# Kernel optimization log

Measured on AMD Instinct MI355X. Metric: run time of the kernel, lower is better.

Reference implementation:

```python
import jax, jax.numpy as jnp
import numpy as np

H = 256          # decoder_size
V = 3            # vocab_size
MAX_LENGTH = 64


def lstm_cell(x, h, c, Wih, Whh, b):
    # PyTorch gate order: i, f, g, o
    g = x @ Wih.T + h @ Whh.T + b
    i, f, gg, o = jnp.split(g, 4, axis=-1)
    c = jax.nn.sigmoid(f) * c + jax.nn.sigmoid(i) * jnp.tanh(gg)
    h = jax.nn.sigmoid(o) * jnp.tanh(c)
    return h, c


def setup_inputs() -> dict:
    key = jax.random.key(0)
    ks = jax.random.split(key, 16)
    T, B, F = 512, 32, 1024
    s = 1.0 / np.sqrt(H)
    u = lambda k, shape: jax.random.uniform(k, shape, jnp.float32, -s, s)
    return dict(
        cnn_feats=jax.random.normal(ks[0], (T, B, F), jnp.float32),
        # bidirectional encoder LSTM (1 layer)
        enc_Wih_f=u(ks[1], (4 * H, F)), enc_Whh_f=u(ks[2], (4 * H, H)), enc_b_f=u(ks[3], (4 * H,)),
        enc_Wih_b=u(ks[4], (4 * H, F)), enc_Whh_b=u(ks[5], (4 * H, H)), enc_b_b=u(ks[6], (4 * H,)),
        # 2-layer decoder LSTM
        dec_Wih0=u(ks[7], (4 * H, H)), dec_Whh0=u(ks[8], (4 * H, H)), dec_b0=u(ks[9], (4 * H,)),
        dec_Wih1=u(ks[10], (4 * H, H)), dec_Whh1=u(ks[11], (4 * H, H)), dec_b1=u(ks[12], (4 * H,)),
        # per-step output projection
        lin_W=u(ks[13], (V, H)), lin_b=u(ks[14], (V,)),
    )


def _forward(cnn_feats, enc_Wih_f, enc_Whh_f, enc_b_f, enc_Wih_b, enc_Whh_b, enc_b_b,
             dec_Wih0, dec_Whh0, dec_b0, dec_Wih1, dec_Whh1, dec_b1, lin_W, lin_b):
    B = cnn_feats.shape[1]
    z = jnp.zeros((B, H), cnn_feats.dtype)

    def run_dir(seq, Wih, Whh, b):
        def step(carry, x):
            h, c = lstm_cell(x, carry[0], carry[1], Wih, Whh, b)
            return (h, c), None
        (h, c), _ = jax.lax.scan(step, (z, z), seq)
        return h, c

    # encoder final states: fwd over seq, bwd over reversed seq
    hf, cf = run_dir(cnn_feats, enc_Wih_f, enc_Whh_f, enc_b_f)
    hb, cb = run_dir(cnn_feats[::-1], enc_Wih_b, enc_Whh_b, enc_b_b)

    # decoder: layer0 init = fwd-dir state, layer1 init = bwd-dir state
    def dstep(carry, _):
        x, h0, c0, h1, c1 = carry
        h0, c0 = lstm_cell(x, h0, c0, dec_Wih0, dec_Whh0, dec_b0)
        h1, c1 = lstm_cell(h0, h1, c1, dec_Wih1, dec_Whh1, dec_b1)
        y = h1 @ lin_W.T + lin_b
        return (h1, h0, c0, h1, c1), y

    _, ys = jax.lax.scan(dstep, (z, hf, cf, hb, cb), None, length=MAX_LENGTH)
    return ys  # (MAX_LENGTH, B, V)


def reference(cnn_feats, enc_Wih_f, enc_Whh_f, enc_b_f, enc_Wih_b, enc_Whh_b, enc_b_b,
              dec_Wih0, dec_Whh0, dec_b0, dec_Wih1, dec_Whh1, dec_b1, lin_W, lin_b):
    return _forward(cnn_feats, enc_Wih_f, enc_Whh_f, enc_b_f, enc_Wih_b, enc_Whh_b, enc_b_b,
                    dec_Wih0, dec_Whh0, dec_b0, dec_Wih1, dec_Whh1, dec_b1, lin_W, lin_b)
```

## Files before the change

kernel.cpp:

```cpp
#include <hip/hip_runtime.h>
#include <stdint.h>
#include <stddef.h>

typedef __attribute__((ext_vector_type(8))) short  short8;
typedef __attribute__((ext_vector_type(4))) float  floatx4;
typedef __attribute__((ext_vector_type(4))) unsigned int u32x4;
typedef unsigned long long u64;

#define SENT 0xAAAAAAAAAAAAAAAAull

static __device__ __forceinline__ float b2f(uint16_t h) {
  union { uint32_t u; float f; } v; v.u = ((uint32_t)h) << 16; return v.f;
}
static __device__ __forceinline__ uint16_t f2b(float f) {
  union { float f; uint32_t u; } v; v.f = f;
  uint32_t u = v.u;
  uint32_t r = u + 0x7FFFu + ((u >> 16) & 1u);
  return (uint16_t)(r >> 16);
}
static __device__ __forceinline__ float sigm(float x)  { return 1.0f / (1.0f + __expf(-x)); }
static __device__ __forceinline__ float tanh_f(float x){ return 1.0f - 2.0f / (1.0f + __expf(2.0f * x)); }

static __device__ __forceinline__ floatx4 mfma16(short8 a, short8 b, floatx4 c) {
  return __builtin_amdgcn_mfma_f32_16x16x32_bf16(a, b, c, 0, 0, 0);
}
static __device__ __forceinline__ short8 cvt8(const float* p) {
  short8 r;
  #pragma unroll
  for (int i = 0; i < 8; ++i) r[i] = (short)f2b(p[i]);
  return r;
}

static __device__ __forceinline__ void st_h64(uint16_t* p, u64 v) {
  __hip_atomic_store((u64*)p, v, __ATOMIC_RELAXED, __HIP_MEMORY_SCOPE_AGENT);
}
static __device__ __forceinline__ u64 ld_h64(const u64* p) {
  return __hip_atomic_load(p, __ATOMIC_RELAXED, __HIP_MEMORY_SCOPE_AGENT);
}
static __device__ __forceinline__ bool frag_ok(u32x4 v) {
  const u64 lo = ((u64)v[1] << 32) | v[0];
  const u64 hi = ((u64)v[3] << 32) | v[2];
  return (lo != SENT) & (hi != SENT);
}
static __device__ __forceinline__ void ld8x16(const uint16_t* p, u32x4* o) {
  asm volatile(
      "global_load_dwordx4 %0, %8, off sc0 sc1\n\t"
      "global_load_dwordx4 %1, %8, off offset:64 sc0 sc1\n\t"
      "global_load_dwordx4 %2, %8, off offset:128 sc0 sc1\n\t"
      "global_load_dwordx4 %3, %8, off offset:192 sc0 sc1\n\t"
      "global_load_dwordx4 %4, %8, off offset:256 sc0 sc1\n\t"
      "global_load_dwordx4 %5, %8, off offset:320 sc0 sc1\n\t"
      "global_load_dwordx4 %6, %8, off offset:384 sc0 sc1\n\t"
      "global_load_dwordx4 %7, %8, off offset:448 sc0 sc1\n\t"
      "s_waitcnt vmcnt(0)"
      : "=&v"(o[0]), "=&v"(o[1]), "=&v"(o[2]), "=&v"(o[3]),
        "=&v"(o[4]), "=&v"(o[5]), "=&v"(o[6]), "=&v"(o[7])
      : "v"(p)
      : "memory");
}
static __device__ __forceinline__ void ld16x16(const uint16_t* pa, const uint16_t* pb,
                                               u32x4* oa, u32x4* ob) {
  asm volatile(
      "global_load_dwordx4 %0, %16, off sc0 sc1\n\t"
      "global_load_dwordx4 %1, %16, off offset:64 sc0 sc1\n\t"
      "global_load_dwordx4 %2, %16, off offset:128 sc0 sc1\n\t"
      "global_load_dwordx4 %3, %16, off offset:192 sc0 sc1\n\t"
      "global_load_dwordx4 %4, %16, off offset:256 sc0 sc1\n\t"
      "global_load_dwordx4 %5, %16, off offset:320 sc0 sc1\n\t"
      "global_load_dwordx4 %6, %16, off offset:384 sc0 sc1\n\t"
      "global_load_dwordx4 %7, %16, off offset:448 sc0 sc1\n\t"
      "global_load_dwordx4 %8, %17, off sc0 sc1\n\t"
      "global_load_dwordx4 %9, %17, off offset:64 sc0 sc1\n\t"
      "global_load_dwordx4 %10, %17, off offset:128 sc0 sc1\n\t"
      "global_load_dwordx4 %11, %17, off offset:192 sc0 sc1\n\t"
      "global_load_dwordx4 %12, %17, off offset:256 sc0 sc1\n\t"
      "global_load_dwordx4 %13, %17, off offset:320 sc0 sc1\n\t"
      "global_load_dwordx4 %14, %17, off offset:384 sc0 sc1\n\t"
      "global_load_dwordx4 %15, %17, off offset:448 sc0 sc1\n\t"
      "s_waitcnt vmcnt(0)"
      : "=&v"(oa[0]), "=&v"(oa[1]), "=&v"(oa[2]), "=&v"(oa[3]),
        "=&v"(oa[4]), "=&v"(oa[5]), "=&v"(oa[6]), "=&v"(oa[7]),
        "=&v"(ob[0]), "=&v"(ob[1]), "=&v"(ob[2]), "=&v"(ob[3]),
        "=&v"(ob[4]), "=&v"(ob[5]), "=&v"(ob[6]), "=&v"(ob[7])
      : "v"(pa), "v"(pb)
      : "memory");
}
static __device__ __forceinline__ void valve8(const uint16_t* p, u32x4* o) {
  const u64* q = (const u64*)p;
  #pragma unroll
  for (int k = 0; k < 8; ++k) {
    u64 a = ld_h64(q + k * 8), c = ld_h64(q + k * 8 + 1);
    o[k][0] = (unsigned)a; o[k][1] = (unsigned)(a >> 32);
    o[k][2] = (unsigned)c; o[k][3] = (unsigned)(c >> 32);
  }
}
static __device__ __forceinline__ void poll8f(const uint16_t* p, u32x4* o) {
  int it = 0;
  for (;;) {
    if ((++it & 1023) == 0) valve8(p, o); else ld8x16(p, o);
    bool ok = true;
    #pragma unroll
    for (int k = 0; k < 8; ++k) ok &= frag_ok(o[k]);
    if (ok) break;
    __builtin_amdgcn_s_sleep(1);
  }
}
static __device__ __forceinline__ void poll16f(const uint16_t* pa, const uint16_t* pb,
                                               u32x4* oa, u32x4* ob) {
  int it = 0;
  for (;;) {
    if ((++it & 1023) == 0) { valve8(pa, oa); valve8(pb, ob); }
    else ld16x16(pa, pb, oa, ob);
    bool ok = true;
    #pragma unroll
    for (int k = 0; k < 8; ++k) ok &= frag_ok(oa[k]) & frag_ok(ob[k]);
    if (ok) break;
    __builtin_amdgcn_s_sleep(1);
  }
}

#define H 256
#define FH 1024
#define BATCH 32
#define TSEQ 512
#define DSTEPS 64
#define ERING 8

__global__ __launch_bounds__(256) void gemm_xw(
    const float* __restrict__ A, const float* __restrict__ W,
    const float* __restrict__ bias, void* __restrict__ Cout, int out_f32)
{
  const int K = 1024, N = 1024;
  __shared__ uint16_t Ah[64 * 40], Al[64 * 40];
  __shared__ uint16_t Wh[64 * 40], Wl[64 * 40];
  const int m0 = blockIdx.x * 64;
  const int n0 = blockIdx.y * 64;
  const int tid = threadIdx.x;
  const int lane = tid & 63, w = tid >> 6;
  const int wm = w & 1, wn = w >> 1;
  const int l15 = lane & 15, q4 = lane >> 4;
  const int ldrow = tid >> 2, ldk = (tid & 3) * 8;

  floatx4 acc[2][2];
  for (int i = 0; i < 2; ++i) for (int j = 0; j < 2; ++j) acc[i][j] = (floatx4){0.f,0.f,0.f,0.f};

  for (int kb = 0; kb < K; kb += 32) {
    float aa[8], ww[8];
    {
      const float4* ap = (const float4*)(A + (size_t)(m0 + ldrow) * K + kb + ldk);
      const float4* wp = (const float4*)(W + (size_t)(n0 + ldrow) * K + kb + ldk);
      *(float4*)(aa) = ap[0]; *(float4*)(aa + 4) = ap[1];
      *(float4*)(ww) = wp[0]; *(float4*)(ww + 4) = wp[1];
    }
    short8 ah, al, wh, wl;
    #pragma unroll
    for (int i = 0; i < 8; ++i) {
      uint16_t h = f2b(aa[i]); ah[i] = (short)h; al[i] = (short)f2b(aa[i] - b2f(h));
      uint16_t g = f2b(ww[i]); wh[i] = (short)g; wl[i] = (short)f2b(ww[i] - b2f(g));
    }
    __syncthreads();
    *(short8*)(Ah + ldrow * 40 + ldk) = ah;
    *(short8*)(Al + ldrow * 40 + ldk) = al;
    *(short8*)(Wh + ldrow * 40 + ldk) = wh;
    *(short8*)(Wl + ldrow * 40 + ldk) = wl;
    __syncthreads();
    short8 afh[2], afl[2], bfh[2], bfl[2];
    #pragma unroll
    for (int mt = 0; mt < 2; ++mt) {
      afh[mt] = *(const short8*)(Ah + (wm * 32 + mt * 16 + l15) * 40 + q4 * 8);
      afl[mt] = *(const short8*)(Al + (wm * 32 + mt * 16 + l15) * 40 + q4 * 8);
    }
    #pragma unroll
    for (int nt = 0; nt < 2; ++nt) {
      bfh[nt] = *(const short8*)(Wh + (wn * 32 + nt * 16 + l15) * 40 + q4 * 8);
      bfl[nt] = *(const short8*)(Wl + (wn * 32 + nt * 16 + l15) * 40 + q4 * 8);
    }
    #pragma unroll
    for (int mt = 0; mt < 2; ++mt)
      #pragma unroll
      for (int nt = 0; nt < 2; ++nt) {
        acc[mt][nt] = mfma16(afh[mt], bfh[nt], acc[mt][nt]);
        acc[mt][nt] = mfma16(afh[mt], bfl[nt], acc[mt][nt]);
        acc[mt][nt] = mfma16(afl[mt], bfh[nt], acc[mt][nt]);
      }
  }
  #pragma unroll
  for (int mt = 0; mt < 2; ++mt)
    #pragma unroll
    for (int nt = 0; nt < 2; ++nt) {
      const int col = n0 + wn * 32 + nt * 16 + l15;
      const float bv = bias[col];
      #pragma unroll
      for (int r = 0; r < 4; ++r) {
        const int row = m0 + wm * 32 + mt * 16 + q4 * 4 + r;
        const float v = acc[mt][nt][r] + bv;
        if (out_f32) ((float*)Cout)[(size_t)row * N + col] = v;
        else         ((uint16_t*)Cout)[(size_t)row * N + col] = f2b(v);
      }
    }
}

__global__ __launch_bounds__(256, 1) void enc_rnn(
    const void* __restrict__ XgF, const void* __restrict__ XgB, int xg_f32,
    const float* __restrict__ WhhF, const float* __restrict__ WhhB,
    uint16_t* __restrict__ hslots,
    uint16_t* __restrict__ hfin, float* __restrict__ cfin)
{
  const int d = blockIdx.x >> 3, q = blockIdx.x & 7;
  const void*  Xg  = d ? XgB : XgF;
  const float* Whh = d ? WhhB : WhhF;
  uint16_t* hsl = hslots + d * (ERING * BATCH * H);
  const int jOff = q * 32;
  const int tid = threadIdx.x, lane = tid & 63, w = tid >> 6;
  const int tt = w & 1, nt = w >> 1, l15 = lane & 15, q4 = lane >> 4;
  const int b = nt * 16 + l15;
  const int jg = jOff + tt * 16 + q4 * 4;

  short8 Af[4][8];
  #pragma unroll
  for (int g = 0; g < 4; ++g) {
    const int grow = g * H + jOff + tt * 16 + l15;
    #pragma unroll
    for (int ks = 0; ks < 8; ++ks)
      Af[g][ks] = cvt8(Whh + (size_t)grow * H + ks * 32 + q4 * 8);
  }

  float cc[4] = {0.f, 0.f, 0.f, 0.f};
  union HV { uint16_t u16[4]; u64 v; } hv; hv.v = 0ull;

  float xvf[16];
  u64   xvb[4];
  auto ldx = [&](int s2) {
    const int t2 = d ? (TSEQ - 1 - s2) : s2;
    const size_t bas = (size_t)(t2 * BATCH + b) * FH + jg;
    if (xg_f32) {
      const float* xp = (const float*)Xg + bas;
      *(float4*)(xvf + 0)  = *(const float4*)(xp);
      *(float4*)(xvf + 4)  = *(const float4*)(xp + H);
      *(float4*)(xvf + 8)  = *(const float4*)(xp + 2 * H);
      *(float4*)(xvf + 12) = *(const float4*)(xp + 3 * H);
    } else {
      const uint16_t* xp = (const uint16_t*)Xg + bas;
      xvb[0] = *(const u64*)(xp);
      xvb[1] = *(const u64*)(xp + H);
      xvb[2] = *(const u64*)(xp + 2 * H);
      xvb[3] = *(const u64*)(xp + 3 * H);
    }
  };
  ldx(0);

  for (int s = 0; s < TSEQ; ++s) {
    floatx4 a0 = {0.f,0.f,0.f,0.f}, a1 = a0, a2 = a0, a3 = a0;
    if (s > 0) {
      u32x4 pol[8];
      const uint16_t* ps = hsl + ((s - 1) & (ERING - 1)) * (BATCH * H) + b * H + q4 * 8;
      poll8f(ps, pol);
      #pragma unroll
      for (int ks = 0; ks < 8; ++ks) {
        short8 bfv = *(short8*)&pol[ks];
        a0 = mfma16(Af[0][ks], bfv, a0);
        a1 = mfma16(Af[1][ks], bfv, a1);
        a2 = mfma16(Af[2][ks], bfv, a2);
        a3 = mfma16(Af[3][ks], bfv, a3);
      }
    }
    #pragma unroll
    for (int r = 0; r < 4; ++r) {
      const float x0 = xg_f32 ? xvf[0 + r]  : b2f((uint16_t)(xvb[0] >> (16 * r)));
      const float x1 = xg_f32 ? xvf[4 + r]  : b2f((uint16_t)(xvb[1] >> (16 * r)));
      const float x2 = xg_f32 ? xvf[8 + r]  : b2f((uint16_t)(xvb[2] >> (16 * r)));
      const float x3 = xg_f32 ? xvf[12 + r] : b2f((uint16_t)(xvb[3] >> (16 * r)));
      const float gi = a0[r] + x0;
      const float gf = a1[r] + x1;
      const float gc = a2[r] + x2;
      const float go = a3[r] + x3;
      const float cn2 = sigm(gf) * cc[r] + sigm(gi) * tanh_f(gc);
      cc[r] = cn2;
      hv.u16[r] = f2b(sigm(go) * tanh_f(cn2));
    }
    st_h64(hsl + (s & (ERING - 1)) * (BATCH * H) + b * H + jg, hv.v);
    if (s >= 6)
      st_h64(hsl + ((s - 6) & (ERING - 1)) * (BATCH * H) + b * H + jg, SENT);
    if (s + 1 < TSEQ) ldx(s + 1);
  }
  #pragma unroll
  for (int r = 0; r < 4; ++r) {
    hfin[d * (BATCH * H) + b * H + jg + r] = hv.u16[r];
    cfin[d * (BATCH * H) + b * H + jg + r] = cc[r];
  }
}

__global__ __launch_bounds__(256, 1) void dec_rnn(
    const float* __restrict__ Wih0, const float* __restrict__ Whh0, const float* __restrict__ bb0,
    const float* __restrict__ Wih1, const float* __restrict__ Whh1, const float* __restrict__ bb1,
    const uint16_t* __restrict__ hfin, const float* __restrict__ cfin,
    uint16_t* __restrict__ h0slots,
    uint16_t* __restrict__ h1slots,
    float*    __restrict__ h1f)
{
  const int L = blockIdx.x >> 3, q = blockIdx.x & 7;
  const float* Wih = L ? Wih1 : Wih0;
  const float* Whh = L ? Whh1 : Whh0;
  const float* bs  = L ? bb1 : bb0;
  const int jOff = q * 32;
  const int tid = threadIdx.x, lane = tid & 63, w = tid >> 6;
  const int tt = w & 1, nt = w >> 1, l15 = lane & 15, q4 = lane >> 4;
  const int b = nt * 16 + l15;
  const int jg = jOff + tt * 16 + q4 * 4;

  short8 Af[4][16];
  #pragma unroll
  for (int g = 0; g < 4; ++g) {
    const int grow = g * H + jOff + tt * 16 + l15;
    #pragma unroll
    for (int ks = 0; ks < 8; ++ks) {
      Af[g][ks]     = cvt8(Wih + (size_t)grow * H + ks * 32 + q4 * 8);
      Af[g][8 + ks] = cvt8(Whh + (size_t)grow * H + ks * 32 + q4 * 8);
    }
  }
  float brg[4][4];
  #pragma unroll
  for (int g = 0; g < 4; ++g)
    #pragma unroll
    for (int r = 0; r < 4; ++r)
      brg[g][r] = bs[g * H + jOff + tt * 16 + q4 * 4 + r];

  float cc[4];
  #pragma unroll
  for (int r = 0; r < 4; ++r) cc[r] = cfin[L * (BATCH * H) + b * H + jg + r];

  uint16_t*       hOwn = L ? h1slots : h0slots;
  const uint16_t* hX   = L ? h0slots : h1slots;
  const int fo = b * H + q4 * 8;
  union HV { uint16_t u16[4]; u64 v; } hv; hv.v = 0ull;

  for (int t = 0; t < DSTEPS; ++t) {
    u32x4 pol[16];
    if (t == 0) {
      const uint16_t* ph = hfin + L * (BATCH * H) + fo;
      #pragma unroll
      for (int k = 0; k < 8; ++k) pol[8 + k] = *(const u32x4*)(ph + k * 32);
      if (L == 0) {
        #pragma unroll
        for (int k = 0; k < 8; ++k) pol[k] = (u32x4){0u, 0u, 0u, 0u};
      } else {
        poll8f(hX + fo, pol);
      }
    } else {
      const uint16_t* pOwn = hOwn + (size_t)(t - 1) * (BATCH * H) + fo;
      const uint16_t* pX   = L ? (hX + (size_t)t * (BATCH * H) + fo)
                               : (hX + (size_t)(t - 1) * (BATCH * H) + fo);
      poll16f(pX, pOwn, pol, pol + 8);
    }

    floatx4 a0 = {0.f,0.f,0.f,0.f}, a1 = a0, a2 = a0, a3 = a0;
    #pragma unroll
    for (int ks = 0; ks < 16; ++ks) {
      short8 bfv = *(short8*)&pol[ks];
      a0 = mfma16(Af[0][ks], bfv, a0);
      a1 = mfma16(Af[1][ks], bfv, a1);
      a2 = mfma16(Af[2][ks], bfv, a2);
      a3 = mfma16(Af[3][ks], bfv, a3);
    }
    float hval[4];
    #pragma unroll
    for (int r = 0; r < 4; ++r) {
      const float gi = a0[r] + brg[0][r];
      const float gf = a1[r] + brg[1][r];
      const float gc = a2[r] + brg[2][r];
      const float go = a3[r] + brg[3][r];
      const float cn2 = sigm(gf) * cc[r] + sigm(gi) * tanh_f(gc);
      cc[r] = cn2;
      hval[r] = sigm(go) * tanh_f(cn2);
      hv.u16[r] = f2b(hval[r]);
    }
    st_h64(hOwn + (size_t)t * (BATCH * H) + b * H + jg, hv.v);
    if (L == 1) {
      float* df = h1f + (size_t)t * (BATCH * H) + b * H + jg;
      #pragma unroll
      for (int r = 0; r < 4; ++r) df[r] = hval[r];
    }
  }
}

__global__ __launch_bounds__(256) void out_proj(
    const float* __restrict__ h1f, const float* __restrict__ linW,
    const float* __restrict__ linb, float* __restrict__ out)
{
  const int idx = blockIdx.x * 256 + threadIdx.x;
  if (idx >= DSTEPS * BATCH * 3) return;
  const int v = idx % 3;
  const int tb = idx / 3;
  const float* hrow = h1f + (size_t)tb * H;
  const float* wrow = linW + (size_t)v * H;
  float s = linb[v];
  for (int k = 0; k < H; ++k) s += hrow[k] * wrow[k];
  out[idx] = s;
}

extern "C" void kernel_launch(void* const* d_in, const int* in_sizes, int n_in,
                              void* d_out, int out_size, void* d_ws, size_t ws_size,
                              hipStream_t stream) {
  (void)in_sizes; (void)n_in; (void)out_size;
  const float* cnn   = (const float*)d_in[0];
  const float* WihF  = (const float*)d_in[1];
  const float* WhhF  = (const float*)d_in[2];
  const float* bF    = (const float*)d_in[3];
  const float* WihB  = (const float*)d_in[4];
  const float* WhhB  = (const float*)d_in[5];
  const float* bB    = (const float*)d_in[6];
  const float* Wih0  = (const float*)d_in[7];
  const float* Whh0  = (const float*)d_in[8];
  const float* b0    = (const float*)d_in[9];
  const float* Wih1  = (const float*)d_in[10];
  const float* Whh1  = (const float*)d_in[11];
  const float* b1    = (const float*)d_in[12];
  const float* linW  = (const float*)d_in[13];
  const float* linb  = (const float*)d_in[14];

  const size_t XG_ELEMS = (size_t)TSEQ * BATCH * FH;
  const size_t SMALL = 2457600;
  const int xg_f32 = (ws_size >= 2 * XG_ELEMS * 4 + SMALL) ? 1 : 0;
  const size_t S = XG_ELEMS * (xg_f32 ? 4 : 2);

  uint8_t* ws = (uint8_t*)d_ws;
  void*     XgF    = (void*)(ws);
  void*     XgB    = (void*)(ws + S);
  float*    h1f    = (float*)(ws + S);
  uint8_t*  base   = ws + 2 * S;
  uint16_t* hslotsE = (uint16_t*)(base);
  uint16_t* h0slots = (uint16_t*)(base + 262144);
  uint16_t* h1slots = (uint16_t*)(base + 1310720);
  uint16_t* hfin    = (uint16_t*)(base + 2359296);
  float*    cfin    = (float*)(base + 2392064);

  hipMemsetAsync(base, 0xAA, 2359296, stream);

  gemm_xw<<<dim3(256, 16), 256, 0, stream>>>(cnn, WihF, bF, XgF, xg_f32);
  gemm_xw<<<dim3(256, 16), 256, 0, stream>>>(cnn, WihB, bB, XgB, xg_f32);
  enc_rnn<<<16, 256, 0, stream>>>(XgF, XgB, xg_f32, WhhF, WhhB,
                                  hslotsE, hfin, cfin);
  dec_rnn<<<16, 256, 0, stream>>>(Wih0, Whh0, b0, Wih1, Whh1, b1,
                                  hfin, cfin, h0slots, h1slots, h1f);
  out_proj<<<24, 256, 0, stream>>>(h1f, linW, linb, (float*)d_out);
}
```

Measured before the change: 2.471 ms.

## Fuse input-projection GEMM into encoder recurrence kernel with per-tile ready flags

```diff
diff --git a/kernel.cpp b/kernel.cpp
--- a/kernel.cpp
+++ b/kernel.cpp
@@ -200,12 +200,99 @@
     }
 }
 
-__global__ __launch_bounds__(256, 1) void enc_rnn(
+__global__ __launch_bounds__(256, 1) void enc_fused(
+    const float* __restrict__ cnn,
+    const float* __restrict__ WihF, const float* __restrict__ bF,
+    const float* __restrict__ WihB, const float* __restrict__ bB,
     const void* __restrict__ XgF, const void* __restrict__ XgB, int xg_f32,
     const float* __restrict__ WhhF, const float* __restrict__ WhhB,
     uint16_t* __restrict__ hslots,
-    uint16_t* __restrict__ hfin, float* __restrict__ cfin)
+    uint16_t* __restrict__ hfin, float* __restrict__ cfin,
+    unsigned int* __restrict__ xgflags)
 {
+  if (blockIdx.x >= 16) {
+    const int K = 1024, N = 1024;
+    __shared__ uint16_t Ah[64 * 40], Al[64 * 40];
+    __shared__ uint16_t Wh[64 * 40], Wl[64 * 40];
+    const int bx = (int)blockIdx.x - 16;
+    const int kk = bx >> 5, sub = bx & 31;
+    const int dirg = sub >> 4, nb = sub & 15;
+    const int mb = dirg ? (255 - kk) : kk;
+    const float* A    = cnn;
+    const float* W    = dirg ? WihB : WihF;
+    const float* bias = dirg ? bB : bF;
+    uint32_t* Co = (uint32_t*)(dirg ? XgB : XgF);
+    const int m0 = mb * 64, n0 = nb * 64;
+    const int tid = threadIdx.x;
+    const int lane = tid & 63, w = tid >> 6;
+    const int wm = w & 1, wn = w >> 1;
+    const int l15 = lane & 15, q4 = lane >> 4;
+    const int ldrow = tid >> 2, ldk = (tid & 3) * 8;
+
+    floatx4 acc[2][2];
+    for (int i = 0; i < 2; ++i) for (int j = 0; j < 2; ++j) acc[i][j] = (floatx4){0.f,0.f,0.f,0.f};
+
+    for (int kb = 0; kb < K; kb += 32) {
+      float aa[8], ww[8];
+      {
+        const float4* ap = (const float4*)(A + (size_t)(m0 + ldrow) * K + kb + ldk);
+        const float4* wp = (const float4*)(W + (size_t)(n0 + ldrow) * K + kb + ldk);
+        *(float4*)(aa) = ap[0]; *(float4*)(aa + 4) = ap[1];
+        *(float4*)(ww) = wp[0]; *(float4*)(ww + 4) = wp[1];
+      }
+      short8 ah, al, wh, wl;
+      #pragma unroll
+      for (int i = 0; i < 8; ++i) {
+        uint16_t h = f2b(aa[i]); ah[i] = (short)h; al[i] = (short)f2b(aa[i] - b2f(h));
+        uint16_t g = f2b(ww[i]); wh[i] = (short)g; wl[i] = (short)f2b(ww[i] - b2f(g));
+      }
+      __syncthreads();
+      *(short8*)(Ah + ldrow * 40 + ldk) = ah;
+      *(short8*)(Al + ldrow * 40 + ldk) = al;
+      *(short8*)(Wh + ldrow * 40 + ldk) = wh;
+      *(short8*)(Wl + ldrow * 40 + ldk) = wl;
+      __syncthreads();
+      short8 afh[2], afl[2], bfh[2], bfl[2];
+      #pragma unroll
+      for (int mt = 0; mt < 2; ++mt) {
+        afh[mt] = *(const short8*)(Ah + (wm * 32 + mt * 16 + l15) * 40 + q4 * 8);
+        afl[mt] = *(const short8*)(Al + (wm * 32 + mt * 16 + l15) * 40 + q4 * 8);
+      }
+      #pragma unroll
+      for (int nt = 0; nt < 2; ++nt) {
+        bfh[nt] = *(const short8*)(Wh + (wn * 32 + nt * 16 + l15) * 40 + q4 * 8);
+        bfl[nt] = *(const short8*)(Wl + (wn * 32 + nt * 16 + l15) * 40 + q4 * 8);
+      }
+      #pragma unroll
+      for (int mt = 0; mt < 2; ++mt)
+        #pragma unroll
+        for (int nt = 0; nt < 2; ++nt) {
+          acc[mt][nt] = mfma16(afh[mt], bfh[nt], acc[mt][nt]);
+          acc[mt][nt] = mfma16(afh[mt], bfl[nt], acc[mt][nt]);
+          acc[mt][nt] = mfma16(afl[mt], bfh[nt], acc[mt][nt]);
+        }
+    }
+    #pragma unroll
+    for (int mt = 0; mt < 2; ++mt)
+      #pragma unroll
+      for (int nt = 0; nt < 2; ++nt) {
+        const int col = n0 + wn * 32 + nt * 16 + l15;
+        const float bv = bias[col];
+        #pragma unroll
+        for (int r = 0; r < 4; ++r) {
+          const int row = m0 + wm * 32 + mt * 16 + q4 * 4 + r;
+          union { float f; uint32_t u; } cv; cv.f = acc[mt][nt][r] + bv;
+          __hip_atomic_store(Co + (size_t)row * N + col, cv.u,
+                             __ATOMIC_RELAXED, __HIP_MEMORY_SCOPE_AGENT);
+        }
+      }
+    __syncthreads();
+    if (threadIdx.x == 0)
+      __hip_atomic_fetch_add(&xgflags[dirg * 256 + mb], 1u,
+                             __ATOMIC_RELEASE, __HIP_MEMORY_SCOPE_AGENT);
+    return;
+  }
+
   const int d = blockIdx.x >> 3, q = blockIdx.x & 7;
   const void*  Xg  = d ? XgB : XgF;
   const float* Whh = d ? WhhB : WhhF;
@@ -227,6 +314,18 @@
 
   float cc[4] = {0.f, 0.f, 0.f, 0.f};
   union HV { uint16_t u16[4]; u64 v; } hv; hv.v = 0ull;
+
+  int mb_prev = -1;
+  auto waitflag = [&](int s2) {
+    const int t2 = d ? (TSEQ - 1 - s2) : s2;
+    const int mb = t2 >> 1;
+    if (mb != mb_prev) {
+      const unsigned int* fp = xgflags + d * 256 + mb;
+      while (__hip_atomic_load(fp, __ATOMIC_ACQUIRE, __HIP_MEMORY_SCOPE_AGENT) < 16u)
+        __builtin_amdgcn_s_sleep(8);
+      mb_prev = mb;
+    }
+  };
 
   float xvf[16];
   u64   xvb[4];
@@ -247,6 +346,7 @@
       xvb[3] = *(const u64*)(xp + 3 * H);
     }
   };
+  waitflag(0);
   ldx(0);
 
   for (int s = 0; s < TSEQ; ++s) {
@@ -281,7 +381,7 @@
     st_h64(hsl + (s & (ERING - 1)) * (BATCH * H) + b * H + jg, hv.v);
     if (s >= 6)
       st_h64(hsl + ((s - 6) & (ERING - 1)) * (BATCH * H) + b * H + jg, SENT);
-    if (s + 1 < TSEQ) ldx(s + 1);
+    if (s + 1 < TSEQ) { waitflag(s + 1); ldx(s + 1); }
   }
   #pragma unroll
   for (int r = 0; r < 4; ++r) {
@@ -419,7 +519,7 @@
   const float* linb  = (const float*)d_in[14];
 
   const size_t XG_ELEMS = (size_t)TSEQ * BATCH * FH;
-  const size_t SMALL = 2457600;
+  const size_t SMALL = 2459648;
   const int xg_f32 = (ws_size >= 2 * XG_ELEMS * 4 + SMALL) ? 1 : 0;
   const size_t S = XG_ELEMS * (xg_f32 ? 4 : 2);
 
@@ -433,13 +533,23 @@
   uint16_t* h1slots = (uint16_t*)(base + 1310720);
   uint16_t* hfin    = (uint16_t*)(base + 2359296);
   float*    cfin    = (float*)(base + 2392064);
+  unsigned int* xgflags = (unsigned int*)(base + 2457600);
 
   hipMemsetAsync(base, 0xAA, 2359296, stream);
 
-  gemm_xw<<<dim3(256, 16), 256, 0, stream>>>(cnn, WihF, bF, XgF, xg_f32);
-  gemm_xw<<<dim3(256, 16), 256, 0, stream>>>(cnn, WihB, bB, XgB, xg_f32);
-  enc_rnn<<<16, 256, 0, stream>>>(XgF, XgB, xg_f32, WhhF, WhhB,
-                                  hslotsE, hfin, cfin);
+  if (xg_f32) {
+    hipMemsetAsync(base + 2457600, 0x00, 2048, stream);
+    enc_fused<<<16 + 8192, 256, 0, stream>>>(
+        cnn, WihF, bF, WihB, bB, XgF, XgB, 1, WhhF, WhhB,
+        hslotsE, hfin, cfin, xgflags);
+  } else {
+    hipMemsetAsync(base + 2457600, 0xFF, 2048, stream);
+    gemm_xw<<<dim3(256, 16), 256, 0, stream>>>(cnn, WihF, bF, XgF, 0);
+    gemm_xw<<<dim3(256, 16), 256, 0, stream>>>(cnn, WihB, bB, XgB, 0);
+    enc_fused<<<16, 256, 0, stream>>>(
+        cnn, WihF, bF, WihB, bB, XgF, XgB, 0, WhhF, WhhB,
+        hslotsE, hfin, cfin, xgflags);
+  }
   dec_rnn<<<16, 256, 0, stream>>>(Wih0, Whh0, b0, Wih1, Whh1, b1,
                                   hfin, cfin, h0slots, h1slots, h1f);
   out_proj<<<24, 256, 0, stream>>>(h1f, linW, linb, (float*)d_out);
```

Measured after the change: 2.345 ms. 1.05x faster.
